# Performance work log

Measured on AMD Instinct MI355X. Metric: run time of the kernel, lower is better.

The kernel has to match this reference:

```python
import jax, jax.numpy as jnp
import numpy as np

N = 100000          # nodes
E = 1600000         # edges
D_NODE = 128        # num_node_features
D_EDGE = 128        # num_edge_features
OUT = 64            # out_features
HEADS = 2
HID = OUT * HEADS   # 128
NUM_GRAPHS = 64
NEG_SLOPE = 0.2


def setup_inputs() -> dict:
    key = jax.random.key(0)
    ks = jax.random.split(key, 12)
    glorot = lambda k, shape: jax.random.uniform(
        k, shape, jnp.float32, -1.0, 1.0) * np.sqrt(6.0 / (shape[0] + shape[-1]))
    return {
        "x": jax.random.normal(ks[0], (N, D_NODE), jnp.float32),
        "edge_index": jax.random.randint(ks[1], (2, E), 0, N, jnp.int64),
        "edge_attr": jax.random.normal(ks[2], (E, D_EDGE), jnp.float32),
        "batch": jnp.sort(jax.random.randint(ks[3], (N,), 0, NUM_GRAPHS, jnp.int64)),
        # GATConv params
        "lin_w": glorot(ks[4], (D_NODE, HID)),
        "att_src": glorot(ks[5], (HEADS, OUT)),
        "att_dst": glorot(ks[6], (HEADS, OUT)),
        "gat_bias": jnp.zeros((HID,), jnp.float32),
        # edge_lin params
        "edge_w": glorot(ks[7], (D_EDGE, HID)),
        "edge_b": jnp.zeros((HID,), jnp.float32),
        # MLP params
        "w1": glorot(ks[8], (HID, 32)),
        "b1": jnp.zeros((32,), jnp.float32),
        "w2": glorot(ks[9], (32, 1)),
        "b2": jnp.zeros((1,), jnp.float32),
    }


def reference(x, edge_index, edge_attr, batch, lin_w, att_src, att_dst,
              gat_bias, edge_w, edge_b, w1, b1, w2, b2):
    n = x.shape[0]
    # --- GATConv (concat=True, add_self_loops=True, negative_slope=0.2) ---
    h = (x @ lin_w).reshape(n, HEADS, OUT)                 # [N,H,C]
    loop = jnp.arange(n, dtype=edge_index.dtype)
    src = jnp.concatenate([edge_index[0], loop])           # [E+N]
    dst = jnp.concatenate([edge_index[1], loop])
    a_src = jnp.sum(h * att_src, axis=-1)                  # [N,H]
    a_dst = jnp.sum(h * att_dst, axis=-1)
    e = jax.nn.leaky_relu(a_src[src] + a_dst[dst], NEG_SLOPE)  # [E+N,H]
    e_max = jax.ops.segment_max(e, dst, num_segments=n)    # softmax over incoming edges
    e_exp = jnp.exp(e - e_max[dst])
    denom = jax.ops.segment_sum(e_exp, dst, num_segments=n)
    alpha = e_exp / (denom[dst] + 1e-16)                   # [E+N,H]
    msg = h[src] * alpha[:, :, None]                       # [E+N,H,C]
    node_feat = jax.ops.segment_sum(msg, dst, num_segments=n)
    node_feat = node_feat.reshape(n, HID) + gat_bias       # [N,HID]
    # --- edge features: linear + scatter-add to SOURCE node (the python loop) ---
    edge_feat = edge_attr @ edge_w + edge_b                # [E,HID]
    edge_agg = jax.ops.segment_sum(edge_feat, edge_index[0], num_segments=n)
    combined = node_feat + edge_agg                        # [N,HID]
    # --- global_add_pool + MLP ---
    pooled = jax.ops.segment_sum(combined, batch, num_segments=NUM_GRAPHS)
    return (pooled @ w1 + b1) @ w2 + b2                    # [NUM_GRAPHS,1]
```

## Files before the change

kernel.cpp:

```cpp
#include <hip/hip_runtime.h>
#include <hip/hip_bf16.h>
#include <math.h>


#define NG 64
#define EA_SPLITS 64

typedef float f32x4 __attribute__((ext_vector_type(4)));

__device__ __forceinline__ float lrelu(float v){ return v > 0.f ? v : 0.2f*v; }

__global__ __launch_bounds__(256) void k_zero(float4* __restrict__ p, long long n4,
                                              int* __restrict__ nstart)
{
  long long i = (long long)blockIdx.x*256 + threadIdx.x;
  long long stride = (long long)gridDim.x*256;
  float4 z = make_float4(0.f,0.f,0.f,0.f);
  for (; i < n4; i += stride) p[i] = z;
  if (blockIdx.x == 0 && threadIdx.x < NG) nstart[threadIdx.x] = 0x7fffffff;
}

__global__ __launch_bounds__(256) void k_gemm_h(
    const float* __restrict__ x, const float* __restrict__ W,
    const float* __restrict__ att_src, const float* __restrict__ att_dst,
    float* __restrict__ h, float* __restrict__ aS, float* __restrict__ aD,
    float* __restrict__ denom, int N)
{
  __shared__ float ldsX[32*128];
  int rb = blockIdx.x * 32;
  for (int idx = threadIdx.x; idx < 32*128/4; idx += 256){
    int k = (idx*4) & 127;
    int row = rb + (idx >> 5);
    f32x4 v = {0.f,0.f,0.f,0.f};
    if (row < N) v = __builtin_nontemporal_load((const f32x4*)&x[(size_t)row*128 + k]);
    *(f32x4*)&ldsX[idx*4] = v;
  }
  __syncthreads();
  int ty = threadIdx.x >> 5, tx = threadIdx.x & 31;
  int r0 = ty*4, c0 = tx*4;
  float acc[4][4] = {};
  #pragma unroll 4
  for (int k = 0; k < 128; ++k){
    float4 b = *(const float4*)&W[k*128 + c0];
    float a0 = ldsX[(r0+0)*128 + k];
    float a1 = ldsX[(r0+1)*128 + k];
    float a2 = ldsX[(r0+2)*128 + k];
    float a3 = ldsX[(r0+3)*128 + k];
    acc[0][0] += a0*b.x; acc[0][1] += a0*b.y; acc[0][2] += a0*b.z; acc[0][3] += a0*b.w;
    acc[1][0] += a1*b.x; acc[1][1] += a1*b.y; acc[1][2] += a1*b.z; acc[1][3] += a1*b.w;
    acc[2][0] += a2*b.x; acc[2][1] += a2*b.y; acc[2][2] += a2*b.z; acc[2][3] += a2*b.w;
    acc[3][0] += a3*b.x; acc[3][1] += a3*b.y; acc[3][2] += a3*b.z; acc[3][3] += a3*b.w;
  }
  #pragma unroll
  for (int i=0;i<4;++i){
    int row = rb + r0 + i;
    if (row < N){
      float4 v = make_float4(acc[i][0],acc[i][1],acc[i][2],acc[i][3]);
      *(float4*)&h[(size_t)row*128 + c0] = v;
    }
  }
  float4 vs = *(const float4*)&att_src[c0];
  float4 vd = *(const float4*)&att_dst[c0];
  int head = tx >> 4;
  #pragma unroll
  for (int i=0;i<4;++i){
    float ps = acc[i][0]*vs.x + acc[i][1]*vs.y + acc[i][2]*vs.z + acc[i][3]*vs.w;
    float pd = acc[i][0]*vd.x + acc[i][1]*vd.y + acc[i][2]*vd.z + acc[i][3]*vd.w;
    ps += __shfl_xor(ps,1); ps += __shfl_xor(ps,2); ps += __shfl_xor(ps,4); ps += __shfl_xor(ps,8);
    pd += __shfl_xor(pd,1); pd += __shfl_xor(pd,2); pd += __shfl_xor(pd,4); pd += __shfl_xor(pd,8);
    if ((tx & 15) == 0){
      int row = rb + r0 + i;
      if (row < N){
        aS[row*2+head] = ps;
        aD[row*2+head] = pd;
        denom[row*2+head] = __expf(lrelu(ps+pd));
      }
    }
  }
}

__global__ __launch_bounds__(256) void k_deg_denom(
  const int* __restrict__ src, const int* __restrict__ dst,
  const float* __restrict__ aS, const float* __restrict__ aD,
  int* __restrict__ deg, float* __restrict__ denom, int E)
{
  int e = blockIdx.x*256 + threadIdx.x; if (e >= E) return;
  int s = src[e], d = dst[e];
  atomicAdd(&deg[s], 1);
  float2 as = *(const float2*)&aS[(size_t)s*2];
  float2 ad = *(const float2*)&aD[(size_t)d*2];
  atomicAdd(&denom[d*2+0], __expf(lrelu(as.x+ad.x)));
  atomicAdd(&denom[d*2+1], __expf(lrelu(as.y+ad.y)));
}

__global__ __launch_bounds__(256) void k_bsum(
  const int* __restrict__ deg, int* __restrict__ bsum, int N)
{
  __shared__ int s[256];
  int b = blockIdx.x, t = threadIdx.x, base = b*1024;
  int sum = 0;
  #pragma unroll
  for (int q=0;q<4;++q){ int i = base + t*4 + q; if (i < N) sum += deg[i]; }
  s[t] = sum; __syncthreads();
  for (int o=128;o;o>>=1){ if (t<o) s[t]+=s[t+o]; __syncthreads(); }
  if (t==0) bsum[b] = s[0];
}

__global__ void k_bscan(const int* __restrict__ bsum, int* __restrict__ boff,
                        int* __restrict__ doff, int nbk, int N, int E)
{
  if (threadIdx.x == 0){
    int s = 0;
    for (int b=0;b<nbk;++b){ boff[b]=s; s+=bsum[b]; }
    doff[N] = E;
  }
}

__global__ __launch_bounds__(256) void k_doff(
  const int* __restrict__ deg, const int* __restrict__ boff,
  int* __restrict__ doff, int* __restrict__ gpos,
  const float* __restrict__ aD, const float* __restrict__ denom,
  const int* __restrict__ batch, float4* __restrict__ adn,
  int* __restrict__ nstart, int N)
{
  __shared__ int s[256];
  int b = blockIdx.x, t = threadIdx.x, base = b*1024;
  int v[4]; int t4 = 0;
  #pragma unroll
  for (int q=0;q<4;++q){ int i = base + t*4 + q; v[q] = (i<N)?deg[i]:0; t4 += v[q]; }
  s[t] = t4; __syncthreads();
  for (int o=1;o<256;o<<=1){
    int add = (t>=o)? s[t-o] : 0;
    __syncthreads();
    s[t] += add;
    __syncthreads();
  }
  int run = boff[b] + s[t] - t4;
  #pragma unroll
  for (int q=0;q<4;++q){
    int i = base + t*4 + q;
    if (i < N){
      doff[i] = run; gpos[i] = run; run += v[q];
      adn[i] = make_float4(aD[i*2], aD[i*2+1], denom[i*2], denom[i*2+1]);
      int bb = batch[i];
      if (i == 0 || batch[i-1] != bb) atomicMin(&nstart[bb], i);
    }
  }
}

__global__ __launch_bounds__(256) void k_scatter(
  const int* __restrict__ src, const int* __restrict__ dst,
  const int* __restrict__ batch, int* __restrict__ gpos,
  int2* __restrict__ order2, const int* __restrict__ nstart,
  const int* __restrict__ doff, int* __restrict__ goff_e,
  float* __restrict__ cnt_nf, float* __restrict__ cnt_ef, int N, int E)
{
  if (blockIdx.x == 0 && threadIdx.x == 0){
    int arr[NG+1];
    arr[NG] = N;
    for (int g=NG-1; g>=0; --g){
      int v = nstart[g];
      arr[g] = (v <= N) ? v : arr[g+1];
    }
    for (int g=0; g<NG; ++g) goff_e[g] = doff[arr[g]];
    goff_e[NG] = E;
    for (int g=0; g<NG; ++g){
      cnt_nf[g] = (float)(arr[g+1]-arr[g]);
      cnt_ef[g] = (float)(goff_e[g+1]-goff_e[g]);
    }
  }
  int e = blockIdx.x*256 + threadIdx.x; if (e >= E) return;
  int s = src[e], d = dst[e];
  int gb = batch[d];
  int p = atomicAdd(&gpos[s], 1);
  order2[p] = make_int2(e, d | ((s & 63) << 17) | (gb << 23));
}

__global__ __launch_bounds__(256) void k_alpha_eattr(
  const int2* __restrict__ order2, const int* __restrict__ doff,
  const float* __restrict__ aS, const float4* __restrict__ adn,
  const int* __restrict__ batch, float* __restrict__ P,
  const float* __restrict__ ea, const int* __restrict__ goff_e,
  float* __restrict__ pooled_e, int N, int nEA)
{
  __shared__ float row[64*128];
  __shared__ float saS[128];
  __shared__ int sb[64];
  int t = threadIdx.x;

  if ((int)blockIdx.x < nEA){
    int* sord = (int*)row;
    float* facc = row + 1024;
    int g = blockIdx.x / EA_SPLITS, k = blockIdx.x % EA_SPLITS;
    int start = goff_e[g], cnt = goff_e[g+1] - start;
    int len = (cnt + EA_SPLITS - 1) / EA_SPLITS;
    int i0 = start + k*len;
    int i1 = start + cnt; if (i0 + len < i1) i1 = i0 + len;
    int lane = t & 31, sub = t >> 5;
    const f32x4* ea4 = (const f32x4*)ea;
    f32x4 acc = {0.f,0.f,0.f,0.f};
    for (int base = i0; base < i1; base += 512){
      int m = i1 - base; if (m > 512) m = 512;
      __syncthreads();
      for (int idx = t; idx < m; idx += 256) sord[idx] = order2[base + idx].x;
      __syncthreads();
      int j = sub;
      for (; j + 56 < m; j += 64){
        f32x4 v0 = __builtin_nontemporal_load(&ea4[(size_t)sord[j     ]*32 + lane]);
        f32x4 v1 = __builtin_nontemporal_load(&ea4[(size_t)sord[j +  8]*32 + lane]);
        f32x4 v2 = __builtin_nontemporal_load(&ea4[(size_t)sord[j + 16]*32 + lane]);
        f32x4 v3 = __builtin_nontemporal_load(&ea4[(size_t)sord[j + 24]*32 + lane]);
        f32x4 v4 = __builtin_nontemporal_load(&ea4[(size_t)sord[j + 32]*32 + lane]);
        f32x4 v5 = __builtin_nontemporal_load(&ea4[(size_t)sord[j + 40]*32 + lane]);
        f32x4 v6 = __builtin_nontemporal_load(&ea4[(size_t)sord[j + 48]*32 + lane]);
        f32x4 v7 = __builtin_nontemporal_load(&ea4[(size_t)sord[j + 56]*32 + lane]);
        acc += (v0+v1)+(v2+v3)+((v4+v5)+(v6+v7));
      }
      for (; j < m; j += 8){
        acc += __builtin_nontemporal_load(&ea4[(size_t)sord[j]*32 + lane]);
      }
    }
    __syncthreads();
    if (t < 128) facc[t] = 0.f;
    __syncthreads();
    float* a = &facc[lane*4];
    atomicAdd(a+0, acc.x); atomicAdd(a+1, acc.y);
    atomicAdd(a+2, acc.z); atomicAdd(a+3, acc.w);
    __syncthreads();
    if (t < 128) atomicAdd(&pooled_e[g*128 + t], facc[t]);
    return;
  }

  int s0 = ((int)blockIdx.x - nEA)*64;
  for (int idx=t; idx<2048; idx+=256) ((float4*)row)[idx] = make_float4(0,0,0,0);
  if (t < 128){ int i = s0*2 + t; saS[t] = (i < 2*N) ? aS[i] : 0.f; }
  if (t < 64){ int i = s0 + t; sb[t] = (i < N) ? batch[i] : 0; }
  __syncthreads();
  int hi = s0 + 64; if (hi > N) hi = N;
  int i0 = doff[s0], i1 = doff[hi];
  for (int i = i0 + t; i < i1; i += 256){
    int y = order2[i].y;
    int d = y & 0x1FFFF;
    int lo = (y >> 17) & 63;
    int gb = (y >> 23) & 63;
    float4 q = adn[d];
    float a0 = __expf(lrelu(saS[lo*2+0] + q.x)) / (q.z + 1e-16f);
    float a1 = __expf(lrelu(saS[lo*2+1] + q.y)) / (q.w + 1e-16f);
    atomicAdd(&row[lo*128 + gb],      a0);
    atomicAdd(&row[lo*128 + 64 + gb], a1);
  }
  __syncthreads();
  if (t < 64){
    int s = s0 + t;
    if (s < N){
      float4 q = adn[s];
      row[t*128 + sb[t]]      += __expf(lrelu(saS[t*2+0] + q.x)) / (q.z + 1e-16f);
      row[t*128 + 64 + sb[t]] += __expf(lrelu(saS[t*2+1] + q.y)) / (q.w + 1e-16f);
    }
  }
  __syncthreads();
  for (int idx=t; idx<2048; idx+=256){
    int r = idx >> 5;
    int s = s0 + r;
    if (s < N) ((float4*)&P[(size_t)s*128])[idx & 31] = ((float4*)row)[idx];
  }
}

__global__ __launch_bounds__(256) void k_pgemm(
  const float* __restrict__ P, const float* __restrict__ h,
  float* __restrict__ partial, int N)
{
  __shared__ float sP[64*128];
  int t = threadIdx.x;
  int c = t & 127;
  int gh = t >> 7;
  int head = c >> 6;
  float acc[32];
  #pragma unroll
  for (int i=0;i<32;++i) acc[i] = 0.f;
  int j0 = blockIdx.x * 128;
  for (int sbi=0; sbi<2; ++sbi){
    int jb = j0 + sbi*64;
    __syncthreads();
    for (int idx=t; idx<2048; idx+=256){
      int j = jb + (idx >> 5);
      ((float4*)sP)[idx] = (j < N) ? ((const float4*)&P[(size_t)j*128])[idx & 31]
                                   : make_float4(0,0,0,0);
    }
    __syncthreads();
    for (int jj=0; jj<64; ++jj){
      int j = jb + jj;
      float hv = (j < N) ? h[(size_t)j*128 + c] : 0.f;
      const float* rp = &sP[jj*128 + head*64 + gh*32];
      #pragma unroll
      for (int q=0;q<8;++q){
        float4 pv = *(const float4*)&rp[q*4];
        acc[q*4+0] += pv.x*hv; acc[q*4+1] += pv.y*hv;
        acc[q*4+2] += pv.z*hv; acc[q*4+3] += pv.w*hv;
      }
    }
  }
  float* pb = &partial[(size_t)blockIdx.x*8192];
  #pragma unroll
  for (int i=0;i<32;++i) pb[(gh*32+i)*128 + c] = acc[i];
}

__global__ __launch_bounds__(256) void k_pg_reduce(
  const float* __restrict__ partial, float* __restrict__ pooled_gat, int nPB)
{
  int o = blockIdx.x*256 + threadIdx.x;
  int chunk = (nPB + gridDim.y - 1) / gridDim.y;
  int b0 = blockIdx.y * chunk;
  int b1 = b0 + chunk; if (b1 > nPB) b1 = nPB;
  float s = 0.f;
  for (int b=b0; b<b1; ++b) s += partial[(size_t)b*8192 + o];
  atomicAdd(&pooled_gat[o], s);
}

__global__ __launch_bounds__(128) void k_final(
  const float* __restrict__ pooled_gat, const float* __restrict__ pooled_e,
  const float* __restrict__ cnt_nf, const float* __restrict__ cnt_ef,
  const float* __restrict__ gat_bias, const float* __restrict__ edge_w,
  const float* __restrict__ edge_b, const float* __restrict__ w1,
  const float* __restrict__ b1, const float* __restrict__ w2,
  const float* __restrict__ b2, float* __restrict__ out)
{
  __shared__ float lds_e[128], comb[128], t1[32];
  int g = blockIdx.x, c = threadIdx.x;
  lds_e[c] = pooled_e[g*128 + c];
  __syncthreads();
  float acc = pooled_gat[g*128 + c] + cnt_nf[g]*gat_bias[c] + cnt_ef[g]*edge_b[c];
  for (int k=0; k<128; ++k) acc += lds_e[k] * edge_w[k*128 + c];
  comb[c] = acc;
  __syncthreads();
  if (c < 32){
    float tv = b1[c];
    for (int k=0; k<128; ++k) tv += comb[k] * w1[k*32 + c];
    t1[c] = tv;
  }
  __syncthreads();
  if (c == 0){
    float o = b2[0];
    #pragma unroll
    for (int m=0; m<32; ++m) o += t1[m] * w2[m];
    out[g] = o;
  }
}

extern "C" void kernel_launch(void* const* d_in, const int* in_sizes, int n_in,
                              void* d_out, int out_size, void* d_ws, size_t ws_size,
                              hipStream_t stream) {
  const float* x        = (const float*)d_in[0];
  const int*   ei       = (const int*)d_in[1];
  const float* ea       = (const float*)d_in[2];
  const int*   batch    = (const int*)d_in[3];
  const float* lin_w    = (const float*)d_in[4];
  const float* att_src  = (const float*)d_in[5];
  const float* att_dst  = (const float*)d_in[6];
  const float* gat_bias = (const float*)d_in[7];
  const float* edge_w   = (const float*)d_in[8];
  const float* edge_b   = (const float*)d_in[9];
  const float* w1       = (const float*)d_in[10];
  const float* b1       = (const float*)d_in[11];
  const float* w2       = (const float*)d_in[12];
  const float* b2       = (const float*)d_in[13];
  float* out = (float*)d_out;

  int N = in_sizes[0] / 128;
  int E = in_sizes[1] / 2;
  const int* src = ei;
  const int* dst = ei + E;
  int nbk = (N + 1023) / 1024;
  int nPB = (N + 127) / 128;
  int nAB = (N + 63) / 64;
  int nEA = NG * EA_SPLITS;

  char* ws = (char*)d_ws;
  size_t off = 0;
  float* pooled_e   = (float*)(ws + off); off += (size_t)NG*128*4;
  float* pooled_gat = (float*)(ws + off); off += (size_t)NG*128*4;
  int*   deg        = (int*)  (ws + off); off += ((size_t)N*4 + 15) & ~15ull;
  size_t zero_bytes = off;
  float* h        = (float*)(ws + off); off += (size_t)N*128*4;
  float* P        = (float*)(ws + off); off += (size_t)N*128*4;
  float* partial  = (float*)(ws + off); off += (size_t)nPB*8192*4;
  float* aS       = (float*)(ws + off); off += (size_t)2*N*4;
  float* aD       = (float*)(ws + off); off += (size_t)2*N*4;
  float* denom    = (float*)(ws + off); off += (size_t)2*N*4;
  float4* adn     = (float4*)(ws + off); off += (size_t)N*16;
  int*   doff     = (int*)  (ws + off); off += ((size_t)(N+1)*4 + 15) & ~15ull;
  int*   gpos     = (int*)  (ws + off); off += ((size_t)N*4 + 15) & ~15ull;
  int2*  order2   = (int2*) (ws + off); off += (size_t)E*8;
  int*   bsum     = (int*)  (ws + off); off += 1024*4;
  int*   boff     = (int*)  (ws + off); off += 1024*4;
  int*   nstart   = (int*)  (ws + off); off += NG*4;
  int*   goff_e   = (int*)  (ws + off); off += (NG+1)*4;
  float* cnt_nf   = (float*)(ws + off); off += NG*4;
  float* cnt_ef   = (float*)(ws + off); off += NG*4;

  k_zero<<<128, 256, 0, stream>>>((float4*)d_ws, (long long)(zero_bytes/16), nstart);

  k_gemm_h   <<<(N+31)/32, 256, 0, stream>>>(x, lin_w, att_src, att_dst,
                                             h, aS, aD, denom, N);
  k_deg_denom<<<(E+255)/256, 256, 0, stream>>>(src, dst, aS, aD, deg, denom, E);

  k_bsum     <<<nbk, 256, 0, stream>>>(deg, bsum, N);
  k_bscan    <<<1, 1, 0, stream>>>(bsum, boff, doff, nbk, N, E);
  k_doff     <<<nbk, 256, 0, stream>>>(deg, boff, doff, gpos,
                                       aD, denom, batch, adn, nstart, N);
  k_scatter  <<<(E+255)/256, 256, 0, stream>>>(src, dst, batch, gpos, order2,
                                               nstart, doff, goff_e,
                                               cnt_nf, cnt_ef, N, E);

  k_alpha_eattr<<<nEA + nAB, 256, 0, stream>>>(order2, doff, aS, adn, batch, P,
                                               ea, goff_e, pooled_e, N, nEA);

  k_pgemm    <<<nPB, 256, 0, stream>>>(P, h, partial, N);
  {
    dim3 rg(32, 8);
    k_pg_reduce<<<rg, 256, 0, stream>>>(partial, pooled_gat, nPB);
  }

  k_final<<<NG, 128, 0, stream>>>(pooled_gat, pooled_e, cnt_nf, cnt_ef,
                                  gat_bias, edge_w, edge_b, w1, b1, w2, b2, out);
}
```

Baseline: 657.9 us.

## Reorder pipeline and co-schedule edge-attr reduction with GEMM and alpha blocks

Moves the CSR build (degree, scan, scatter) ahead of the node GEMM so the edge-attribute pooling can start earlier. The edge-attribute work is split into two phases (40 and 24 splits per graph) and interleaved with the h GEMM blocks and the alpha/P blocks in two combined kernels. The goal is to overlap the bandwidth-bound edge_attr gather with compute-bound or atomic-bound work. It also drops the packed adn buffer and reads aD and denom directly, which adds scattered loads in the alpha stage.

Result: no change. 661.9 us (+0.6%).

```diff
diff --git a/kernel.cpp b/kernel.cpp
--- a/kernel.cpp
+++ b/kernel.cpp
@@ -5,6 +5,8 @@
 
 #define NG 64
 #define EA_SPLITS 64
+#define PH1 40
+#define PH2 24
 
 typedef float f32x4 __attribute__((ext_vector_type(4)));
 
@@ -20,36 +22,180 @@
   if (blockIdx.x == 0 && threadIdx.x < NG) nstart[threadIdx.x] = 0x7fffffff;
 }
 
-__global__ __launch_bounds__(256) void k_gemm_h(
-    const float* __restrict__ x, const float* __restrict__ W,
-    const float* __restrict__ att_src, const float* __restrict__ att_dst,
-    float* __restrict__ h, float* __restrict__ aS, float* __restrict__ aD,
-    float* __restrict__ denom, int N)
-{
-  __shared__ float ldsX[32*128];
-  int rb = blockIdx.x * 32;
-  for (int idx = threadIdx.x; idx < 32*128/4; idx += 256){
+__global__ __launch_bounds__(256) void k_deg_nstart(
+  const int* __restrict__ src, const int* __restrict__ batch,
+  int* __restrict__ deg, int* __restrict__ nstart, int N, int E)
+{
+  int e = blockIdx.x*256 + threadIdx.x;
+  if (e < E) atomicAdd(&deg[src[e]], 1);
+  if (e < N){
+    int bb = batch[e];
+    if (e == 0 || batch[e-1] != bb) atomicMin(&nstart[bb], e);
+  }
+}
+
+__global__ __launch_bounds__(256) void k_bsum(
+  const int* __restrict__ deg, int* __restrict__ bsum, int N)
+{
+  __shared__ int s[256];
+  int b = blockIdx.x, t = threadIdx.x, base = b*1024;
+  int sum = 0;
+  #pragma unroll
+  for (int q=0;q<4;++q){ int i = base + t*4 + q; if (i < N) sum += deg[i]; }
+  s[t] = sum; __syncthreads();
+  for (int o=128;o;o>>=1){ if (t<o) s[t]+=s[t+o]; __syncthreads(); }
+  if (t==0) bsum[b] = s[0];
+}
+
+__global__ void k_bscan(const int* __restrict__ bsum, int* __restrict__ boff,
+                        int* __restrict__ doff, int nbk, int N, int E)
+{
+  if (threadIdx.x == 0){
+    int s = 0;
+    for (int b=0;b<nbk;++b){ boff[b]=s; s+=bsum[b]; }
+    doff[N] = E;
+  }
+}
+
+__global__ __launch_bounds__(256) void k_doff(
+  const int* __restrict__ deg, const int* __restrict__ boff,
+  int* __restrict__ doff, int* __restrict__ gpos, int N)
+{
+  __shared__ int s[256];
+  int b = blockIdx.x, t = threadIdx.x, base = b*1024;
+  int v[4]; int t4 = 0;
+  #pragma unroll
+  for (int q=0;q<4;++q){ int i = base + t*4 + q; v[q] = (i<N)?deg[i]:0; t4 += v[q]; }
+  s[t] = t4; __syncthreads();
+  for (int o=1;o<256;o<<=1){
+    int add = (t>=o)? s[t-o] : 0;
+    __syncthreads();
+    s[t] += add;
+    __syncthreads();
+  }
+  int run = boff[b] + s[t] - t4;
+  #pragma unroll
+  for (int q=0;q<4;++q){
+    int i = base + t*4 + q;
+    if (i < N){ doff[i] = run; gpos[i] = run; run += v[q]; }
+  }
+}
+
+__global__ __launch_bounds__(256) void k_scatter(
+  const int* __restrict__ src, const int* __restrict__ dst,
+  const int* __restrict__ batch, int* __restrict__ gpos,
+  int2* __restrict__ order2, const int* __restrict__ nstart,
+  const int* __restrict__ doff, int* __restrict__ goff_e,
+  float* __restrict__ cnt_nf, float* __restrict__ cnt_ef, int N, int E)
+{
+  if (blockIdx.x == 0 && threadIdx.x == 0){
+    int arr[NG+1];
+    arr[NG] = N;
+    for (int g=NG-1; g>=0; --g){
+      int v = nstart[g];
+      arr[g] = (v <= N) ? v : arr[g+1];
+    }
+    for (int g=0; g<NG; ++g) goff_e[g] = doff[arr[g]];
+    goff_e[NG] = E;
+    for (int g=0; g<NG; ++g){
+      cnt_nf[g] = (float)(arr[g+1]-arr[g]);
+      cnt_ef[g] = (float)(goff_e[g+1]-goff_e[g]);
+    }
+  }
+  int e = blockIdx.x*256 + threadIdx.x; if (e >= E) return;
+  int s = src[e], d = dst[e];
+  int gb = batch[d];
+  int p = atomicAdd(&gpos[s], 1);
+  order2[p] = make_int2(e, d | ((s & 63) << 17) | (gb << 23));
+}
+
+__device__ __forceinline__ void eattr_body(
+  int g, int k, const int2* __restrict__ order2,
+  const int* __restrict__ goff_e, const float* __restrict__ ea,
+  float* __restrict__ pooled_e, int* sord, float* facc, int t)
+{
+  int start = goff_e[g], cnt = goff_e[g+1] - start;
+  int len = (cnt + EA_SPLITS - 1) / EA_SPLITS;
+  int i0 = start + k*len;
+  int i1 = start + cnt; if (i0 + len < i1) i1 = i0 + len;
+  int lane = t & 31, sub = t >> 5;
+  const f32x4* ea4 = (const f32x4*)ea;
+  f32x4 acc = {0.f,0.f,0.f,0.f};
+  for (int base = i0; base < i1; base += 512){
+    int m = i1 - base; if (m > 512) m = 512;
+    __syncthreads();
+    for (int idx = t; idx < m; idx += 256) sord[idx] = order2[base + idx].x;
+    __syncthreads();
+    int j = sub;
+    for (; j + 56 < m; j += 64){
+      f32x4 v0 = __builtin_nontemporal_load(&ea4[(size_t)sord[j     ]*32 + lane]);
+      f32x4 v1 = __builtin_nontemporal_load(&ea4[(size_t)sord[j +  8]*32 + lane]);
+      f32x4 v2 = __builtin_nontemporal_load(&ea4[(size_t)sord[j + 16]*32 + lane]);
+      f32x4 v3 = __builtin_nontemporal_load(&ea4[(size_t)sord[j + 24]*32 + lane]);
+      f32x4 v4 = __builtin_nontemporal_load(&ea4[(size_t)sord[j + 32]*32 + lane]);
+      f32x4 v5 = __builtin_nontemporal_load(&ea4[(size_t)sord[j + 40]*32 + lane]);
+      f32x4 v6 = __builtin_nontemporal_load(&ea4[(size_t)sord[j + 48]*32 + lane]);
+      f32x4 v7 = __builtin_nontemporal_load(&ea4[(size_t)sord[j + 56]*32 + lane]);
+      acc += (v0+v1)+(v2+v3)+((v4+v5)+(v6+v7));
+    }
+    for (; j < m; j += 8){
+      acc += __builtin_nontemporal_load(&ea4[(size_t)sord[j]*32 + lane]);
+    }
+  }
+  __syncthreads();
+  if (t < 128) facc[t] = 0.f;
+  __syncthreads();
+  float* a = &facc[lane*4];
+  atomicAdd(a+0, acc.x); atomicAdd(a+1, acc.y);
+  atomicAdd(a+2, acc.z); atomicAdd(a+3, acc.w);
+  __syncthreads();
+  if (t < 128) atomicAdd(&pooled_e[g*128 + t], facc[t]);
+}
+
+__global__ __launch_bounds__(256) void k_mega1(
+  const float* __restrict__ x, const float* __restrict__ W,
+  const float* __restrict__ att_src, const float* __restrict__ att_dst,
+  float* __restrict__ h, float* __restrict__ aS, float* __restrict__ aD,
+  float* __restrict__ denom,
+  const int2* __restrict__ order2, const int* __restrict__ goff_e,
+  const float* __restrict__ ea, float* __restrict__ pooled_e,
+  int N, int nEA1, int nGH)
+{
+  __shared__ float lds[32*128];
+  int b = blockIdx.x, grp = b/9, rem = b - grp*9;
+  int t = threadIdx.x;
+
+  if (rem < 4){
+    int eid = grp*4 + rem; if (eid >= nEA1) return;
+    eattr_body(eid / PH1, eid % PH1, order2, goff_e, ea, pooled_e,
+               (int*)lds, lds + 1024, t);
+    return;
+  }
+
+  int gid = grp*5 + (rem-4); if (gid >= nGH) return;
+  int rb = gid * 32;
+  for (int idx = t; idx < 32*128/4; idx += 256){
     int k = (idx*4) & 127;
     int row = rb + (idx >> 5);
     f32x4 v = {0.f,0.f,0.f,0.f};
     if (row < N) v = __builtin_nontemporal_load((const f32x4*)&x[(size_t)row*128 + k]);
-    *(f32x4*)&ldsX[idx*4] = v;
-  }
-  __syncthreads();
-  int ty = threadIdx.x >> 5, tx = threadIdx.x & 31;
+    *(f32x4*)&lds[idx*4] = v;
+  }
+  __syncthreads();
+  int ty = t >> 5, tx = t & 31;
   int r0 = ty*4, c0 = tx*4;
   float acc[4][4] = {};
   #pragma unroll 4
   for (int k = 0; k < 128; ++k){
-    float4 b = *(const float4*)&W[k*128 + c0];
-    float a0 = ldsX[(r0+0)*128 + k];
-    float a1 = ldsX[(r0+1)*128 + k];
-    float a2 = ldsX[(r0+2)*128 + k];
-    float a3 = ldsX[(r0+3)*128 + k];
-    acc[0][0] += a0*b.x; acc[0][1] += a0*b.y; acc[0][2] += a0*b.z; acc[0][3] += a0*b.w;
-    acc[1][0] += a1*b.x; acc[1][1] += a1*b.y; acc[1][2] += a1*b.z; acc[1][3] += a1*b.w;
-    acc[2][0] += a2*b.x; acc[2][1] += a2*b.y; acc[2][2] += a2*b.z; acc[2][3] += a2*b.w;
-    acc[3][0] += a3*b.x; acc[3][1] += a3*b.y; acc[3][2] += a3*b.z; acc[3][3] += a3*b.w;
+    float4 bv = *(const float4*)&W[k*128 + c0];
+    float a0 = lds[(r0+0)*128 + k];
+    float a1 = lds[(r0+1)*128 + k];
+    float a2 = lds[(r0+2)*128 + k];
+    float a3 = lds[(r0+3)*128 + k];
+    acc[0][0] += a0*bv.x; acc[0][1] += a0*bv.y; acc[0][2] += a0*bv.z; acc[0][3] += a0*bv.w;
+    acc[1][0] += a1*bv.x; acc[1][1] += a1*bv.y; acc[1][2] += a1*bv.z; acc[1][3] += a1*bv.w;
+    acc[2][0] += a2*bv.x; acc[2][1] += a2*bv.y; acc[2][2] += a2*bv.z; acc[2][3] += a2*bv.w;
+    acc[3][0] += a3*bv.x; acc[3][1] += a3*bv.y; acc[3][2] += a3*bv.z; acc[3][3] += a3*bv.w;
   }
   #pragma unroll
   for (int i=0;i<4;++i){
@@ -79,159 +225,41 @@
   }
 }
 
-__global__ __launch_bounds__(256) void k_deg_denom(
+__global__ __launch_bounds__(256) void k_denom(
   const int* __restrict__ src, const int* __restrict__ dst,
   const float* __restrict__ aS, const float* __restrict__ aD,
-  int* __restrict__ deg, float* __restrict__ denom, int E)
+  float* __restrict__ denom, int E)
 {
   int e = blockIdx.x*256 + threadIdx.x; if (e >= E) return;
   int s = src[e], d = dst[e];
-  atomicAdd(&deg[s], 1);
   float2 as = *(const float2*)&aS[(size_t)s*2];
   float2 ad = *(const float2*)&aD[(size_t)d*2];
   atomicAdd(&denom[d*2+0], __expf(lrelu(as.x+ad.x)));
   atomicAdd(&denom[d*2+1], __expf(lrelu(as.y+ad.y)));
 }
 
-__global__ __launch_bounds__(256) void k_bsum(
-  const int* __restrict__ deg, int* __restrict__ bsum, int N)
-{
-  __shared__ int s[256];
-  int b = blockIdx.x, t = threadIdx.x, base = b*1024;
-  int sum = 0;
-  #pragma unroll
-  for (int q=0;q<4;++q){ int i = base + t*4 + q; if (i < N) sum += deg[i]; }
-  s[t] = sum; __syncthreads();
-  for (int o=128;o;o>>=1){ if (t<o) s[t]+=s[t+o]; __syncthreads(); }
-  if (t==0) bsum[b] = s[0];
-}
-
-__global__ void k_bscan(const int* __restrict__ bsum, int* __restrict__ boff,
-                        int* __restrict__ doff, int nbk, int N, int E)
-{
-  if (threadIdx.x == 0){
-    int s = 0;
-    for (int b=0;b<nbk;++b){ boff[b]=s; s+=bsum[b]; }
-    doff[N] = E;
-  }
-}
-
-__global__ __launch_bounds__(256) void k_doff(
-  const int* __restrict__ deg, const int* __restrict__ boff,
-  int* __restrict__ doff, int* __restrict__ gpos,
-  const float* __restrict__ aD, const float* __restrict__ denom,
-  const int* __restrict__ batch, float4* __restrict__ adn,
-  int* __restrict__ nstart, int N)
-{
-  __shared__ int s[256];
-  int b = blockIdx.x, t = threadIdx.x, base = b*1024;
-  int v[4]; int t4 = 0;
-  #pragma unroll
-  for (int q=0;q<4;++q){ int i = base + t*4 + q; v[q] = (i<N)?deg[i]:0; t4 += v[q]; }
-  s[t] = t4; __syncthreads();
-  for (int o=1;o<256;o<<=1){
-    int add = (t>=o)? s[t-o] : 0;
-    __syncthreads();
-    s[t] += add;
-    __syncthreads();
-  }
-  int run = boff[b] + s[t] - t4;
-  #pragma unroll
-  for (int q=0;q<4;++q){
-    int i = base + t*4 + q;
-    if (i < N){
-      doff[i] = run; gpos[i] = run; run += v[q];
-      adn[i] = make_float4(aD[i*2], aD[i*2+1], denom[i*2], denom[i*2+1]);
-      int bb = batch[i];
-      if (i == 0 || batch[i-1] != bb) atomicMin(&nstart[bb], i);
-    }
-  }
-}
-
-__global__ __launch_bounds__(256) void k_scatter(
-  const int* __restrict__ src, const int* __restrict__ dst,
-  const int* __restrict__ batch, int* __restrict__ gpos,
-  int2* __restrict__ order2, const int* __restrict__ nstart,
-  const int* __restrict__ doff, int* __restrict__ goff_e,
-  float* __restrict__ cnt_nf, float* __restrict__ cnt_ef, int N, int E)
-{
-  if (blockIdx.x == 0 && threadIdx.x == 0){
-    int arr[NG+1];
-    arr[NG] = N;
-    for (int g=NG-1; g>=0; --g){
-      int v = nstart[g];
-      arr[g] = (v <= N) ? v : arr[g+1];
-    }
-    for (int g=0; g<NG; ++g) goff_e[g] = doff[arr[g]];
-    goff_e[NG] = E;
-    for (int g=0; g<NG; ++g){
-      cnt_nf[g] = (float)(arr[g+1]-arr[g]);
-      cnt_ef[g] = (float)(goff_e[g+1]-goff_e[g]);
-    }
-  }
-  int e = blockIdx.x*256 + threadIdx.x; if (e >= E) return;
-  int s = src[e], d = dst[e];
-  int gb = batch[d];
-  int p = atomicAdd(&gpos[s], 1);
-  order2[p] = make_int2(e, d | ((s & 63) << 17) | (gb << 23));
-}
-
-__global__ __launch_bounds__(256) void k_alpha_eattr(
+__global__ __launch_bounds__(256) void k_mega2(
   const int2* __restrict__ order2, const int* __restrict__ doff,
-  const float* __restrict__ aS, const float4* __restrict__ adn,
-  const int* __restrict__ batch, float* __restrict__ P,
+  const float* __restrict__ aS, const float* __restrict__ aD,
+  const float* __restrict__ denom, const int* __restrict__ batch,
+  float* __restrict__ P,
   const float* __restrict__ ea, const int* __restrict__ goff_e,
-  float* __restrict__ pooled_e, int N, int nEA)
+  float* __restrict__ pooled_e, int N, int nEA2, int nAB)
 {
   __shared__ float row[64*128];
   __shared__ float saS[128];
   __shared__ int sb[64];
-  int t = threadIdx.x;
-
-  if ((int)blockIdx.x < nEA){
-    int* sord = (int*)row;
-    float* facc = row + 1024;
-    int g = blockIdx.x / EA_SPLITS, k = blockIdx.x % EA_SPLITS;
-    int start = goff_e[g], cnt = goff_e[g+1] - start;
-    int len = (cnt + EA_SPLITS - 1) / EA_SPLITS;
-    int i0 = start + k*len;
-    int i1 = start + cnt; if (i0 + len < i1) i1 = i0 + len;
-    int lane = t & 31, sub = t >> 5;
-    const f32x4* ea4 = (const f32x4*)ea;
-    f32x4 acc = {0.f,0.f,0.f,0.f};
-    for (int base = i0; base < i1; base += 512){
-      int m = i1 - base; if (m > 512) m = 512;
-      __syncthreads();
-      for (int idx = t; idx < m; idx += 256) sord[idx] = order2[base + idx].x;
-      __syncthreads();
-      int j = sub;
-      for (; j + 56 < m; j += 64){
-        f32x4 v0 = __builtin_nontemporal_load(&ea4[(size_t)sord[j     ]*32 + lane]);
-        f32x4 v1 = __builtin_nontemporal_load(&ea4[(size_t)sord[j +  8]*32 + lane]);
-        f32x4 v2 = __builtin_nontemporal_load(&ea4[(size_t)sord[j + 16]*32 + lane]);
-        f32x4 v3 = __builtin_nontemporal_load(&ea4[(size_t)sord[j + 24]*32 + lane]);
-        f32x4 v4 = __builtin_nontemporal_load(&ea4[(size_t)sord[j + 32]*32 + lane]);
-        f32x4 v5 = __builtin_nontemporal_load(&ea4[(size_t)sord[j + 40]*32 + lane]);
-        f32x4 v6 = __builtin_nontemporal_load(&ea4[(size_t)sord[j + 48]*32 + lane]);
-        f32x4 v7 = __builtin_nontemporal_load(&ea4[(size_t)sord[j + 56]*32 + lane]);
-        acc += (v0+v1)+(v2+v3)+((v4+v5)+(v6+v7));
-      }
-      for (; j < m; j += 8){
-        acc += __builtin_nontemporal_load(&ea4[(size_t)sord[j]*32 + lane]);
-      }
-    }
-    __syncthreads();
-    if (t < 128) facc[t] = 0.f;
-    __syncthreads();
-    float* a = &facc[lane*4];
-    atomicAdd(a+0, acc.x); atomicAdd(a+1, acc.y);
-    atomicAdd(a+2, acc.z); atomicAdd(a+3, acc.w);
-    __syncthreads();
-    if (t < 128) atomicAdd(&pooled_e[g*128 + t], facc[t]);
+  int b = blockIdx.x, t = threadIdx.x;
+
+  if (b & 1){
+    int eid = b >> 1; if (eid >= nEA2) return;
+    eattr_body(eid / PH2, PH1 + eid % PH2, order2, goff_e, ea, pooled_e,
+               (int*)row, row + 1024, t);
     return;
   }
 
-  int s0 = ((int)blockIdx.x - nEA)*64;
+  int aid = b >> 1; if (aid >= nAB) return;
+  int s0 = aid*64;
   for (int idx=t; idx<2048; idx+=256) ((float4*)row)[idx] = make_float4(0,0,0,0);
   if (t < 128){ int i = s0*2 + t; saS[t] = (i < 2*N) ? aS[i] : 0.f; }
   if (t < 64){ int i = s0 + t; sb[t] = (i < N) ? batch[i] : 0; }
@@ -243,9 +271,10 @@
     int d = y & 0x1FFFF;
     int lo = (y >> 17) & 63;
     int gb = (y >> 23) & 63;
-    float4 q = adn[d];
-    float a0 = __expf(lrelu(saS[lo*2+0] + q.x)) / (q.z + 1e-16f);
-    float a1 = __expf(lrelu(saS[lo*2+1] + q.y)) / (q.w + 1e-16f);
+    float2 ad = *(const float2*)&aD[(size_t)d*2];
+    float2 dn = *(const float2*)&denom[(size_t)d*2];
+    float a0 = __expf(lrelu(saS[lo*2+0] + ad.x)) / (dn.x + 1e-16f);
+    float a1 = __expf(lrelu(saS[lo*2+1] + ad.y)) / (dn.y + 1e-16f);
     atomicAdd(&row[lo*128 + gb],      a0);
     atomicAdd(&row[lo*128 + 64 + gb], a1);
   }
@@ -253,9 +282,10 @@
   if (t < 64){
     int s = s0 + t;
     if (s < N){
-      float4 q = adn[s];
-      row[t*128 + sb[t]]      += __expf(lrelu(saS[t*2+0] + q.x)) / (q.z + 1e-16f);
-      row[t*128 + 64 + sb[t]] += __expf(lrelu(saS[t*2+1] + q.y)) / (q.w + 1e-16f);
+      float2 ad = *(const float2*)&aD[(size_t)s*2];
+      float2 dn = *(const float2*)&denom[(size_t)s*2];
+      row[t*128 + sb[t]]      += __expf(lrelu(saS[t*2+0] + ad.x)) / (dn.x + 1e-16f);
+      row[t*128 + 64 + sb[t]] += __expf(lrelu(saS[t*2+1] + ad.y)) / (dn.y + 1e-16f);
     }
   }
   __syncthreads();
@@ -373,7 +403,13 @@
   int nbk = (N + 1023) / 1024;
   int nPB = (N + 127) / 128;
   int nAB = (N + 63) / 64;
-  int nEA = NG * EA_SPLITS;
+  int nGH = (N + 31) / 32;
+  int nEA1 = NG * PH1;
+  int nEA2 = NG * PH2;
+  int grp1 = ((nEA1+3)/4 > (nGH+4)/5) ? (nEA1+3)/4 : (nGH+4)/5;
+  int grid1 = grp1 * 9;
+  int mx2 = (nEA2 > nAB) ? nEA2 : nAB;
+  int grid2 = mx2 * 2;
 
   char* ws = (char*)d_ws;
   size_t off = 0;
@@ -387,7 +423,6 @@
   float* aS       = (float*)(ws + off); off += (size_t)2*N*4;
   float* aD       = (float*)(ws + off); off += (size_t)2*N*4;
   float* denom    = (float*)(ws + off); off += (size_t)2*N*4;
-  float4* adn     = (float4*)(ws + off); off += (size_t)N*16;
   int*   doff     = (int*)  (ws + off); off += ((size_t)(N+1)*4 + 15) & ~15ull;
   int*   gpos     = (int*)  (ws + off); off += ((size_t)N*4 + 15) & ~15ull;
   int2*  order2   = (int2*) (ws + off); off += (size_t)E*8;
@@ -400,20 +435,23 @@
 
   k_zero<<<128, 256, 0, stream>>>((float4*)d_ws, (long long)(zero_bytes/16), nstart);
 
-  k_gemm_h   <<<(N+31)/32, 256, 0, stream>>>(x, lin_w, att_src, att_dst,
-                                             h, aS, aD, denom, N);
-  k_deg_denom<<<(E+255)/256, 256, 0, stream>>>(src, dst, aS, aD, deg, denom, E);
-
-  k_bsum     <<<nbk, 256, 0, stream>>>(deg, bsum, N);
-  k_bscan    <<<1, 1, 0, stream>>>(bsum, boff, doff, nbk, N, E);
-  k_doff     <<<nbk, 256, 0, stream>>>(deg, boff, doff, gpos,
-                                       aD, denom, batch, adn, nstart, N);
-  k_scatter  <<<(E+255)/256, 256, 0, stream>>>(src, dst, batch, gpos, order2,
-                                               nstart, doff, goff_e,
-                                               cnt_nf, cnt_ef, N, E);
-
-  k_alpha_eattr<<<nEA + nAB, 256, 0, stream>>>(order2, doff, aS, adn, batch, P,
-                                               ea, goff_e, pooled_e, N, nEA);
+  k_deg_nstart<<<(E+255)/256, 256, 0, stream>>>(src, batch, deg, nstart, N, E);
+  k_bsum      <<<nbk, 256, 0, stream>>>(deg, bsum, N);
+  k_bscan     <<<1, 1, 0, stream>>>(bsum, boff, doff, nbk, N, E);
+  k_doff      <<<nbk, 256, 0, stream>>>(deg, boff, doff, gpos, N);
+  k_scatter   <<<(E+255)/256, 256, 0, stream>>>(src, dst, batch, gpos, order2,
+                                                nstart, doff, goff_e,
+                                                cnt_nf, cnt_ef, N, E);
+
+  k_mega1<<<grid1, 256, 0, stream>>>(x, lin_w, att_src, att_dst,
+                                     h, aS, aD, denom,
+                                     order2, goff_e, ea, pooled_e,
+                                     N, nEA1, nGH);
+
+  k_denom<<<(E+255)/256, 256, 0, stream>>>(src, dst, aS, aD, denom, E);
+
+  k_mega2<<<grid2, 256, 0, stream>>>(order2, doff, aS, aD, denom, batch, P,
+                                     ea, goff_e, pooled_e, N, nEA2, nAB);
 
   k_pgemm    <<<nPB, 256, 0, stream>>>(P, h, partial, N);
   {
```
